# Optimization experiments

Hardware: AMD Instinct MI355X
Metric: run time of the kernel (lower is better)

## Reference

```python
import jax, jax.numpy as jnp
import numpy as np

IN_C = 256
QK_C = IN_C // 8  # 32
B, H, W = 8, 64, 64


def setup_inputs() -> dict:
    key = jax.random.key(0)
    ks = jax.random.split(key, 8)
    s_in = 1.0 / np.sqrt(IN_C)
    return {
        "x": jax.random.normal(ks[0], (B, IN_C, H, W), dtype=jnp.float32),
        "Wq": jax.random.normal(ks[1], (QK_C, IN_C), dtype=jnp.float32) * s_in,
        "bq": jax.random.normal(ks[2], (QK_C,), dtype=jnp.float32) * 0.01,
        "Wk": jax.random.normal(ks[3], (QK_C, IN_C), dtype=jnp.float32) * s_in,
        "bk": jax.random.normal(ks[4], (QK_C,), dtype=jnp.float32) * 0.01,
        "Wv": jax.random.normal(ks[5], (IN_C, IN_C), dtype=jnp.float32) * s_in,
        "bv": jax.random.normal(ks[6], (IN_C,), dtype=jnp.float32) * 0.01,
        # gamma is init to zero in the module, but use nonzero so output depends on attention
        "gamma": jnp.full((1,), 0.5, dtype=jnp.float32),
    }


def reference(x, Wq, bq, Wk, bk, Wv, bv, gamma):
    b, c, h, w = x.shape
    n = h * w
    xf = x.reshape(b, c, n)  # [B, C, N]
    # 1x1 convs == per-pixel linear projections over channels
    q = jnp.einsum('dc,bcn->bdn', Wq, xf) + bq[None, :, None]  # [B, C//8, N]
    k = jnp.einsum('dc,bcn->bdn', Wk, xf) + bk[None, :, None]  # [B, C//8, N]
    v = jnp.einsum('oc,bcn->bon', Wv, xf) + bv[None, :, None]  # [B, C, N]
    # attention_map[b, m, n'] = softmax_n'( q[b,:,m] . k[b,:,n'] )
    scores = jnp.einsum('bdm,bdn->bmn', q, k)  # [B, N, N]
    attn = jax.nn.softmax(scores, axis=-1)
    # out[b,c,m] = sum_n v[b,c,n] * attn[b,m,n]
    out = jnp.einsum('bcn,bmn->bcm', v, attn).reshape(b, c, h, w)
    return gamma * out + x
```

## Files before the change

### kernel.cpp

```cpp
#include <hip/hip_runtime.h>
#include <cstdint>

typedef __bf16 bf16x8 __attribute__((ext_vector_type(8)));
typedef float f32x16 __attribute__((ext_vector_type(16)));

#define LOG2E 1.44269504088896340736f

static __device__ __forceinline__ ushort f2bf(float f) {
  uint u = __builtin_bit_cast(uint, f);
  u = u + 0x7FFFu + ((u >> 16) & 1u);
  return (ushort)(u >> 16);
}

static __device__ __forceinline__ uint cvtpk_bf16(float lo, float hi) {
  uint r;
  asm("v_cvt_pk_bf16_f32 %0, %1, %2" : "=v"(r) : "v"(lo), "v"(hi));
  return r;
}

static __device__ __forceinline__ void plswap(uint& a, uint& b) {
  asm("v_permlane32_swap_b32 %0, %1" : "+v"(a), "+v"(b));
}

static __device__ __forceinline__ void gload16(const ushort* g, ushort* l) {
  __builtin_amdgcn_global_load_lds(
      (const __attribute__((address_space(1))) void*)g,
      (__attribute__((address_space(3))) void*)l, 16, 0, 0);
}

#if __has_builtin(__builtin_amdgcn_exp2f)
#define EXP2(x) __builtin_amdgcn_exp2f(x)
#else
#define EXP2(x) exp2f(x)
#endif


__global__ __launch_bounds__(256, 2) void proj_qkv(
    const float* __restrict__ x,
    const float* __restrict__ Wq, const float* __restrict__ bq,
    const float* __restrict__ Wk, const float* __restrict__ bk,
    const float* __restrict__ Wv, const float* __restrict__ bv,
    ushort* __restrict__ qo, ushort* __restrict__ ko, ushort* __restrict__ vo)
{
  __shared__ __align__(16) union SM {
    ushort xc[2][8192];
    ushort qT[256 * 40];
  } sm;

  const int tid = threadIdx.x;
  const int nt = blockIdx.x, b = blockIdx.y, dt = blockIdx.z;
  const int n0 = nt * 256;
  const int wv = tid >> 6, lane = tid & 63;
  const int l31 = lane & 31, hi = lane >> 5;
  const int dh = wv & 1, nh = wv >> 1;

  const float* wrow;
  float wsc = 1.0f;
  if (dt == 0) {
    if (dh == 0) { wrow = Wq + (size_t)l31 * 256; wsc = LOG2E; }
    else         { wrow = Wk + (size_t)l31 * 256; }
  } else {
    wrow = Wv + (size_t)((dt - 1) * 64 + dh * 32 + l31) * 256;
  }
  bf16x8 wf[16];
#pragma unroll
  for (int s = 0; s < 16; ++s) {
    float4 a = *(const float4*)(wrow + s * 16 + 8 * hi);
    float4 c = *(const float4*)(wrow + s * 16 + 8 * hi + 4);
    union { uint u[4]; bf16x8 v; } t;
    t.u[0] = cvtpk_bf16(a.x * wsc, a.y * wsc);
    t.u[1] = cvtpk_bf16(a.z * wsc, a.w * wsc);
    t.u[2] = cvtpk_bf16(c.x * wsc, c.y * wsc);
    t.u[3] = cvtpk_bf16(c.z * wsc, c.w * wsc);
    wf[s] = t.v;
  }

  f32x16 acc[4];
#pragma unroll
  for (int Tl = 0; Tl < 4; ++Tl)
#pragma unroll
    for (int r = 0; r < 16; ++r) acc[Tl][r] = 0.f;

  const float* xb = x + (size_t)b * 256 * 4096;

  const int o = wv, qd = lane;
  float4 xr[8];

  auto XLOAD = [&](int kc) {
    const float* src = xb + (size_t)(kc * 32 + 8 * o) * 4096 + n0 + 4 * qd;
#pragma unroll
    for (int j = 0; j < 8; ++j) xr[j] = *(const float4*)(src + (size_t)j * 4096);
  };
  auto XWRITE = [&](int buf) {
    const int base = (qd >> 3) * 1024 + (o >> 1) * 512 + (o & 1) * 256 + (qd & 7) * 32;
    const int xsw = (qd & 6) << 2;
#pragma unroll
    for (int e = 0; e < 4; ++e) {
      uint4 w;
      w.x = cvtpk_bf16(xr[0][e], xr[1][e]);
      w.y = cvtpk_bf16(xr[2][e], xr[3][e]);
      w.z = cvtpk_bf16(xr[4][e], xr[5][e]);
      w.w = cvtpk_bf16(xr[6][e], xr[7][e]);
      *(uint4*)&sm.xc[buf][(base + e * 8) ^ xsw] = w;
    }
  };

  const int rdoff = (lane * 8) ^ (((l31 >> 2) & 6) << 2);

  XLOAD(0);
  asm volatile("s_waitcnt vmcnt(0)" ::: "memory");
  XWRITE(0);
  __syncthreads();

  for (int kc = 0; kc < 8; ++kc) {
    if (kc < 7) XLOAD(kc + 1);
    const ushort* buf = sm.xc[kc & 1];
#pragma unroll
    for (int s2 = 0; s2 < 2; ++s2) {
#pragma unroll
      for (int Tl = 0; Tl < 4; ++Tl) {
        const int T = nh * 4 + Tl;
        bf16x8 a = *(const bf16x8*)&buf[T * 1024 + s2 * 512 + rdoff];
        if (s2 == 0)
          acc[Tl] = __builtin_amdgcn_mfma_f32_32x32x16_bf16(a, wf[kc * 2 + 0], acc[Tl], 0, 0, 0);
        else
          acc[Tl] = __builtin_amdgcn_mfma_f32_32x32x16_bf16(a, wf[kc * 2 + 1], acc[Tl], 0, 0, 0);
      }
    }
    if (kc < 7) {
      asm volatile("s_waitcnt vmcnt(0)" ::: "memory");
      XWRITE((kc + 1) & 1);
    }
    __syncthreads();
  }

  if (dt == 0) {
    if (dh == 0) {
      const float bq_ = bq[l31] * LOG2E;
#pragma unroll
      for (int Tl = 0; Tl < 4; ++Tl)
#pragma unroll
        for (int r = 0; r < 16; ++r) {
          int nl = (nh * 4 + Tl) * 32 + (r & 3) + 8 * (r >> 2) + 4 * hi;
          sm.qT[nl * 40 + l31] = f2bf(acc[Tl][r] + bq_);
        }
    } else {
      const float bk_ = bk[l31];
      const int kd = l31;
      const size_t kzb = (size_t)b * 131072;
      const size_t dbase = (size_t)(kd >> 4) * 512 + ((kd >> 3) & 1) * 256 + (kd & 7);
#pragma unroll
      for (int Tl = 0; Tl < 4; ++Tl) {
        const size_t Tg = (size_t)(nt * 8 + nh * 4 + Tl);
#pragma unroll
        for (int r = 0; r < 16; ++r) {
          int n31 = (r & 3) + 8 * (r >> 2) + 4 * hi;
          ko[kzb + Tg * 1024 + dbase + (size_t)n31 * 8] = f2bf(acc[Tl][r] + bk_);
        }
      }
    }
    __syncthreads();
    {
      ushort* dst = qo + (size_t)b * 131072 + (size_t)(n0 + tid) * 32;
#pragma unroll
      for (int i = 0; i < 4; ++i)
        *(uint4*)(dst + i * 8) = *(const uint4*)&sm.qT[tid * 40 + i * 8];
    }
  } else {
    const float bv_ = bv[(dt - 1) * 64 + dh * 32 + l31];
    const int cu = (dt - 1) * 2 + dh;
    const size_t vzb = (size_t)b * 1048576;
#pragma unroll
    for (int Tl = 0; Tl < 4; ++Tl) {
      const size_t Tg = (size_t)(nt * 8 + nh * 4 + Tl);
#pragma unroll
      for (int g = 0; g < 4; ++g) {
        ushort4 w;
        w.x = f2bf(acc[Tl][g * 4 + 0] + bv_);
        w.y = f2bf(acc[Tl][g * 4 + 1] + bv_);
        w.z = f2bf(acc[Tl][g * 4 + 2] + bv_);
        w.w = f2bf(acc[Tl][g * 4 + 3] + bv_);
        size_t addr = vzb + Tg * 8192 + (size_t)(cu * 2 + (g >> 1)) * 512
                      + (size_t)(g & 1) * 256 + (size_t)l31 * 8 + 4 * hi;
        *(ushort4*)(vo + addr) = w;
      }
    }
  }
}

static __device__ __forceinline__ float softmax_pack_only(
    f32x16& s, float& mrun, float& lsum, bf16x8& pb0o, bf16x8& pb1o)
{
  float pm = s[0];
#pragma unroll
  for (int r = 1; r < 16; ++r) pm = fmaxf(pm, s[r]);
  pm = fmaxf(pm, __shfl_xor(pm, 32));

  float aa = 1.0f;
  if (!__all(pm <= mrun + 8.0f)) {
    float mnew = fmaxf(mrun, pm);
    aa = EXP2(mrun - mnew);
    mrun = mnew;
    lsum *= aa;
  }

  float p[16];
  float ps = 0.f;
#pragma unroll
  for (int r = 0; r < 16; ++r) { p[r] = EXP2(s[r] - mrun); ps += p[r]; }
  ps += __shfl_xor(ps, 32);
  lsum += ps;

  uint pw[8];
#pragma unroll
  for (int j = 0; j < 8; ++j) pw[j] = cvtpk_bf16(p[2 * j], p[2 * j + 1]);
  plswap(pw[0], pw[2]); plswap(pw[1], pw[3]);
  plswap(pw[4], pw[6]); plswap(pw[5], pw[7]);
  union { uint u[4]; bf16x8 v; } pb0u, pb1u;
  pb0u.u[0] = pw[0]; pb0u.u[1] = pw[1]; pb0u.u[2] = pw[2]; pb0u.u[3] = pw[3];
  pb1u.u[0] = pw[4]; pb1u.u[1] = pw[5]; pb1u.u[2] = pw[6]; pb1u.u[3] = pw[7];
  pb0o = pb0u.v; pb1o = pb1u.v;
  return aa;
}

__global__ __launch_bounds__(512, 2) void attn_fused(
    const ushort* __restrict__ qs, const ushort* __restrict__ kz,
    const ushort* __restrict__ vz, const float* __restrict__ x,
    const float* __restrict__ gamma, float* __restrict__ out)
{
  __shared__ __align__(16) union SMem {
    ushort vbuf[8][2][2048];
    float  xch[4][2][2][16][64];
  } sm;
  __shared__ __align__(16) ushort kbuf[2][4][1024];
  __shared__ uint  pexch[2][2][4][64][8];
  __shared__ float afac[2][2][4][64];
  __shared__ float mlbuf[2][4][2][64];

  const int wg = blockIdx.x;
  const int swz = (wg & 7) * 32 + (wg >> 3);
  const int b = swz >> 5, mt = swz & 31;
  const int tid = threadIdx.x;
  const int wv = tid >> 6, lane = tid & 63;
  const int kh = wv >> 2, q = wv & 3;
  const int l31 = lane & 31, hi = lane >> 5;
  const int mbase = mt * 128;
  const int mSelf = mbase + q * 32 + l31;

  const ushort* qrow = qs + (size_t)b * 131072 + (size_t)mSelf * 32;
  bf16x8 qf0 = *(const bf16x8*)(qrow + 8 * hi);
  bf16x8 qf1 = *(const bf16x8*)(qrow + 16 + 8 * hi);

  const ushort* kb = kz + (size_t)b * 131072 + (size_t)kh * 64 * 1024;
  const ushort* vb = vz + (size_t)b * 1048576 + (size_t)kh * 64 * 8192;

  f32x16 acc[4][2];
#pragma unroll
  for (int mu = 0; mu < 4; ++mu)
#pragma unroll
    for (int cf = 0; cf < 2; ++cf)
#pragma unroll
      for (int r = 0; r < 16; ++r) acc[mu][cf][r] = 0.f;

  const f32x16 fzero = {};
  float mrun = -1e30f, lsum = 0.f;

  const int pswz = (lane * 8) ^ (lane & 4);

  auto ISSUE_V = [&](int t, int par) {
#pragma unroll
    for (int i = 0; i < 4; ++i)
      gload16(vb + (size_t)t * 8192 + (size_t)(q * 4 + i) * 512 + lane * 8,
              &sm.vbuf[wv][par][i * 512]);
  };
  auto ISSUE_K = [&](int t) {
    if (q < 2)
      gload16(kb + (size_t)t * 1024 + (size_t)q * 512 + lane * 8,
              &kbuf[kh][t & 3][q * 512]);
  };

  ISSUE_V(0, 0);
  ISSUE_K(0);
  ISSUE_K(1);
  ISSUE_V(1, 1);
  ISSUE_K(2);
  if (q < 2) { asm volatile("s_waitcnt vmcnt(5)" ::: "memory"); }
  else       { asm volatile("s_waitcnt vmcnt(4)" ::: "memory"); }
  __builtin_amdgcn_s_barrier();

#define BODY(T, W01, W23)                                                      \
  {                                                                            \
    const int t_ = (T);                                                        \
    const int vpar = t_ & 1, kslot = t_ & 3, xpar = t_ & 1;                    \
    if (q < 2) { asm volatile("s_waitcnt vmcnt(" #W01 ")" ::: "memory"); }     \
    else       { asm volatile("s_waitcnt vmcnt(" #W23 ")" ::: "memory"); }     \
                                                          \
    bf16x8 ka0 = *(const bf16x8*)&kbuf[kh][kslot][lane * 8];                   \
    bf16x8 ka1 = *(const bf16x8*)&kbuf[kh][kslot][512 + lane * 8];             \
    f32x16 s = __builtin_amdgcn_mfma_f32_32x32x16_bf16(ka0, qf0, fzero, 0, 0, 0); \
    s = __builtin_amdgcn_mfma_f32_32x32x16_bf16(ka1, qf1, s, 0, 0, 0);         \
    bf16x8 pbS0, pbS1;                                                         \
    float aa = softmax_pack_only(s, mrun, lsum, pbS0, pbS1);                   \
    { union { bf16x8 v; uint4 u; } c0, c1; c0.v = pbS0; c1.v = pbS1;           \
      uint* pp = &pexch[kh][xpar][q][0][0];                                    \
      *(uint4*)(pp + pswz) = c0.u;                                             \
      *(uint4*)(pp + (pswz ^ 4)) = c1.u; }                                     \
    afac[kh][xpar][q][lane] = aa;                                              \
    asm volatile("s_waitcnt lgkmcnt(0)" ::: "memory");                         \
    __builtin_amdgcn_s_barrier();                                              \
                                      \
    bf16x8 va0 = *(const bf16x8*)&sm.vbuf[wv][vpar][0 * 512 + lane * 8];       \
    bf16x8 va1 = *(const bf16x8*)&sm.vbuf[wv][vpar][1 * 512 + lane * 8];       \
    bf16x8 va2 = *(const bf16x8*)&sm.vbuf[wv][vpar][2 * 512 + lane * 8];       \
    bf16x8 va3 = *(const bf16x8*)&sm.vbuf[wv][vpar][3 * 512 + lane * 8];       \
    _Pragma("unroll")                                                          \
    for (int mu = 0; mu < 4; ++mu) {                                           \
      float aaU = afac[kh][xpar][mu][lane];                                    \
      uint* pr = &pexch[kh][xpar][mu][0][0];                                   \
      union { uint4 u; bf16x8 v; } r0, r1;                                     \
      r0.u = *(const uint4*)(pr + pswz);                                       \
      r1.u = *(const uint4*)(pr + (pswz ^ 4));                                 \
      if (!__all(aaU == 1.0f)) {                                               \
        _Pragma("unroll")                                                      \
        for (int cf = 0; cf < 2; ++cf)                                         \
          _Pragma("unroll")                                                    \
          for (int r = 0; r < 16; ++r) acc[mu][cf][r] *= aaU;                  \
      }                                                                        \
      __builtin_amdgcn_s_setprio(1);                                           \
      acc[mu][0] = __builtin_amdgcn_mfma_f32_32x32x16_bf16(va0, r0.v, acc[mu][0], 0, 0, 0); \
      acc[mu][0] = __builtin_amdgcn_mfma_f32_32x32x16_bf16(va1, r1.v, acc[mu][0], 0, 0, 0); \
      acc[mu][1] = __builtin_amdgcn_mfma_f32_32x32x16_bf16(va2, r0.v, acc[mu][1], 0, 0, 0); \
      acc[mu][1] = __builtin_amdgcn_mfma_f32_32x32x16_bf16(va3, r1.v, acc[mu][1], 0, 0, 0); \
      __builtin_amdgcn_s_setprio(0);                                           \
    }                                                                          \
    if (t_ < 62) ISSUE_V(t_ + 2, vpar);                                        \
    if (t_ < 61) ISSUE_K(t_ + 3);                                              \
  }

  for (int t = 0; t < 62; ++t) BODY(t, 5, 4);
  BODY(62, 4, 4);
  BODY(63, 0, 0);
#undef BODY

  mlbuf[kh][q][0][lane] = mrun;
  mlbuf[kh][q][1][lane] = lsum;
  asm volatile("s_waitcnt lgkmcnt(0)" ::: "memory");
  __builtin_amdgcn_s_barrier();

  const float g = gamma[0];
  const float* xc = x + (size_t)b * 256 * 4096;
  float* oc = out + (size_t)b * 256 * 4096;

  if (kh == 1) {
#pragma unroll
    for (int mu = 0; mu < 2; ++mu)
#pragma unroll
      for (int cf = 0; cf < 2; ++cf)
#pragma unroll
        for (int r = 0; r < 16; ++r)
          sm.xch[q][mu][cf][r][lane] = acc[mu][cf][r];
  }
  asm volatile("s_waitcnt lgkmcnt(0)" ::: "memory");
  __builtin_amdgcn_s_barrier();
  if (kh == 0) {
#pragma unroll
    for (int mu = 0; mu < 2; ++mu) {
      float m0 = mlbuf[0][mu][0][lane], l0 = mlbuf[0][mu][1][lane];
      float m1 = mlbuf[1][mu][0][lane], l1 = mlbuf[1][mu][1][lane];
      float ms = fmaxf(m0, m1);
      float w0 = EXP2(m0 - ms), w1 = EXP2(m1 - ms);
      float inv = 1.0f / (l0 * w0 + l1 * w1);
      int m = mbase + mu * 32 + l31;
#pragma unroll
      for (int cf = 0; cf < 2; ++cf)
#pragma unroll
        for (int r = 0; r < 16; ++r) {
          float val = acc[mu][cf][r] * w0 + sm.xch[q][mu][cf][r][lane] * w1;
          int c = q * 64 + cf * 32 + (r & 3) + 8 * (r >> 2) + 4 * hi;
          oc[(size_t)c * 4096 + m] = g * (val * inv) + xc[(size_t)c * 4096 + m];
        }
    }
  }
  __builtin_amdgcn_s_barrier();
  if (kh == 1) {
#pragma unroll
    for (int mu = 0; mu < 2; ++mu)
#pragma unroll
      for (int cf = 0; cf < 2; ++cf)
#pragma unroll
        for (int r = 0; r < 16; ++r)
          sm.xch[q][mu][cf][r][lane] = acc[2 + mu][cf][r];
  }
  asm volatile("s_waitcnt lgkmcnt(0)" ::: "memory");
  __builtin_amdgcn_s_barrier();
  if (kh == 0) {
#pragma unroll
    for (int mu = 0; mu < 2; ++mu) {
      float m0 = mlbuf[0][2 + mu][0][lane], l0 = mlbuf[0][2 + mu][1][lane];
      float m1 = mlbuf[1][2 + mu][0][lane], l1 = mlbuf[1][2 + mu][1][lane];
      float ms = fmaxf(m0, m1);
      float w0 = EXP2(m0 - ms), w1 = EXP2(m1 - ms);
      float inv = 1.0f / (l0 * w0 + l1 * w1);
      int m = mbase + (2 + mu) * 32 + l31;
#pragma unroll
      for (int cf = 0; cf < 2; ++cf)
#pragma unroll
        for (int r = 0; r < 16; ++r) {
          float val = acc[2 + mu][cf][r] * w0 + sm.xch[q][mu][cf][r][lane] * w1;
          int c = q * 64 + cf * 32 + (r & 3) + 8 * (r >> 2) + 4 * hi;
          oc[(size_t)c * 4096 + m] = g * (val * inv) + xc[(size_t)c * 4096 + m];
        }
    }
  }
}

extern "C" void kernel_launch(void* const* d_in, const int* in_sizes, int n_in,
                              void* d_out, int out_size, void* d_ws, size_t ws_size,
                              hipStream_t stream) {
  const float* x  = (const float*)d_in[0];
  const float* Wq = (const float*)d_in[1];
  const float* bq = (const float*)d_in[2];
  const float* Wk = (const float*)d_in[3];
  const float* bk = (const float*)d_in[4];
  const float* Wv = (const float*)d_in[5];
  const float* bv = (const float*)d_in[6];
  const float* gm = (const float*)d_in[7];
  float* out = (float*)d_out;

  ushort* qs = (ushort*)d_ws;
  ushort* kzp = qs + (size_t)8 * 131072;
  ushort* vzp = kzp + (size_t)8 * 131072;

  proj_qkv<<<dim3(16, 8, 5), 256, 0, stream>>>(x, Wq, bq, Wk, bk, Wv, bv, qs, kzp, vzp);
  attn_fused<<<dim3(256), 512, 0, stream>>>(qs, kzp, vzp, x, gm, out);
}
```

Baseline: 138.7 us.

## Software-pipeline PV of previous tile with QK softmax of current tile

Restructures the attention loop so each iteration computes the QK scores for tile t and then runs the PV matmul for tile t-1, before the softmax of tile t. This overlaps the softmax's exp/ALU work and barrier latency with MFMA work from the previous tile, collapsing to one barrier per iteration. The V prefetch distance shrinks from two tiles ahead to one, the vmcnt waits are retuned, and sched_barriers are added to pin the instruction order. The risk is that the shorter V prefetch exposes load latency, and the fixed scheduling may block useful compiler reordering.

```diff
diff --git a/kernel.cpp b/kernel.cpp
--- a/kernel.cpp
+++ b/kernel.cpp
@@ -279,44 +279,24 @@
               &kbuf[kh][t & 3][q * 512]);
   };
 
-  ISSUE_V(0, 0);
   ISSUE_K(0);
   ISSUE_K(1);
-  ISSUE_V(1, 1);
+  ISSUE_V(0, 0);
   ISSUE_K(2);
-  if (q < 2) { asm volatile("s_waitcnt vmcnt(5)" ::: "memory"); }
-  else       { asm volatile("s_waitcnt vmcnt(4)" ::: "memory"); }
+  if (q < 2) { asm volatile("s_waitcnt vmcnt(1)" ::: "memory"); }
   __builtin_amdgcn_s_barrier();
-
-#define BODY(T, W01, W23)                                                      \
+  __builtin_amdgcn_sched_barrier(0);
+
+#define PV_PREV(SLOT)                                                          \
   {                                                                            \
-    const int t_ = (T);                                                        \
-    const int vpar = t_ & 1, kslot = t_ & 3, xpar = t_ & 1;                    \
-    if (q < 2) { asm volatile("s_waitcnt vmcnt(" #W01 ")" ::: "memory"); }     \
-    else       { asm volatile("s_waitcnt vmcnt(" #W23 ")" ::: "memory"); }     \
-                                                          \
-    bf16x8 ka0 = *(const bf16x8*)&kbuf[kh][kslot][lane * 8];                   \
-    bf16x8 ka1 = *(const bf16x8*)&kbuf[kh][kslot][512 + lane * 8];             \
-    f32x16 s = __builtin_amdgcn_mfma_f32_32x32x16_bf16(ka0, qf0, fzero, 0, 0, 0); \
-    s = __builtin_amdgcn_mfma_f32_32x32x16_bf16(ka1, qf1, s, 0, 0, 0);         \
-    bf16x8 pbS0, pbS1;                                                         \
-    float aa = softmax_pack_only(s, mrun, lsum, pbS0, pbS1);                   \
-    { union { bf16x8 v; uint4 u; } c0, c1; c0.v = pbS0; c1.v = pbS1;           \
-      uint* pp = &pexch[kh][xpar][q][0][0];                                    \
-      *(uint4*)(pp + pswz) = c0.u;                                             \
-      *(uint4*)(pp + (pswz ^ 4)) = c1.u; }                                     \
-    afac[kh][xpar][q][lane] = aa;                                              \
-    asm volatile("s_waitcnt lgkmcnt(0)" ::: "memory");                         \
-    __builtin_amdgcn_s_barrier();                                              \
-                                      \
-    bf16x8 va0 = *(const bf16x8*)&sm.vbuf[wv][vpar][0 * 512 + lane * 8];       \
-    bf16x8 va1 = *(const bf16x8*)&sm.vbuf[wv][vpar][1 * 512 + lane * 8];       \
-    bf16x8 va2 = *(const bf16x8*)&sm.vbuf[wv][vpar][2 * 512 + lane * 8];       \
-    bf16x8 va3 = *(const bf16x8*)&sm.vbuf[wv][vpar][3 * 512 + lane * 8];       \
+    bf16x8 va0 = *(const bf16x8*)&sm.vbuf[wv][SLOT][0 * 512 + lane * 8];       \
+    bf16x8 va1 = *(const bf16x8*)&sm.vbuf[wv][SLOT][1 * 512 + lane * 8];       \
+    bf16x8 va2 = *(const bf16x8*)&sm.vbuf[wv][SLOT][2 * 512 + lane * 8];       \
+    bf16x8 va3 = *(const bf16x8*)&sm.vbuf[wv][SLOT][3 * 512 + lane * 8];       \
     _Pragma("unroll")                                                          \
     for (int mu = 0; mu < 4; ++mu) {                                           \
-      float aaU = afac[kh][xpar][mu][lane];                                    \
-      uint* pr = &pexch[kh][xpar][mu][0][0];                                   \
+      float aaU = afac[kh][SLOT][mu][lane];                                    \
+      uint* pr = &pexch[kh][SLOT][mu][0][0];                                   \
       union { uint4 u; bf16x8 v; } r0, r1;                                     \
       r0.u = *(const uint4*)(pr + pswz);                                       \
       r1.u = *(const uint4*)(pr + (pswz ^ 4));                                 \
@@ -333,19 +313,50 @@
       acc[mu][1] = __builtin_amdgcn_mfma_f32_32x32x16_bf16(va3, r1.v, acc[mu][1], 0, 0, 0); \
       __builtin_amdgcn_s_setprio(0);                                           \
     }                                                                          \
-    if (t_ < 62) ISSUE_V(t_ + 2, vpar);                                        \
-    if (t_ < 61) ISSUE_K(t_ + 3);                                              \
-  }
-
-  for (int t = 0; t < 62; ++t) BODY(t, 5, 4);
-  BODY(62, 4, 4);
-  BODY(63, 0, 0);
+  }
+
+#define BODY(T, W01, W23, DO_PV)                                               \
+  {                                                                            \
+    const int t_ = (T);                                                        \
+    const int kslot = t_ & 3, xpar = t_ & 1, slotP = (t_ ^ 1) & 1;             \
+    if (q < 2) { asm volatile("s_waitcnt vmcnt(" #W01 ")" ::: "memory"); }     \
+    else       { asm volatile("s_waitcnt vmcnt(" #W23 ")" ::: "memory"); }     \
+                               \
+    bf16x8 ka0 = *(const bf16x8*)&kbuf[kh][kslot][lane * 8];                   \
+    bf16x8 ka1 = *(const bf16x8*)&kbuf[kh][kslot][512 + lane * 8];             \
+    f32x16 s = __builtin_amdgcn_mfma_f32_32x32x16_bf16(ka0, qf0, fzero, 0, 0, 0); \
+    s = __builtin_amdgcn_mfma_f32_32x32x16_bf16(ka1, qf1, s, 0, 0, 0);         \
+        \
+    if (DO_PV) PV_PREV(slotP);                                                 \
+    bf16x8 pbS0, pbS1;                                                         \
+    float aa = softmax_pack_only(s, mrun, lsum, pbS0, pbS1);                   \
+    { union { bf16x8 v; uint4 u; } c0, c1; c0.v = pbS0; c1.v = pbS1;           \
+      uint* pp = &pexch[kh][xpar][q][0][0];                                    \
+      *(uint4*)(pp + pswz) = c0.u;                                             \
+      *(uint4*)(pp + (pswz ^ 4)) = c1.u; }                                     \
+    afac[kh][xpar][q][lane] = aa;                                              \
+    asm volatile("s_waitcnt lgkmcnt(0)" ::: "memory");                         \
+    __builtin_amdgcn_s_barrier();                                              \
+    __builtin_amdgcn_sched_barrier(0);                                         \
+          \
+    if (t_ <= 62) ISSUE_V(t_ + 1, slotP);                                      \
+    if (t_ <= 60) ISSUE_K(t_ + 3);                                             \
+  }
+
+  BODY(0, 20, 20, false);
+  for (int t = 1; t < 62; ++t) BODY(t, 5, 4, true);
+  BODY(62, 4, 4, true);
+  BODY(63, 4, 4, true);
 #undef BODY
+  asm volatile("s_waitcnt vmcnt(0)" ::: "memory");
+  PV_PREV(1);
+#undef PV_PREV
 
   mlbuf[kh][q][0][lane] = mrun;
   mlbuf[kh][q][1][lane] = lsum;
   asm volatile("s_waitcnt lgkmcnt(0)" ::: "memory");
   __builtin_amdgcn_s_barrier();
+  __builtin_amdgcn_sched_barrier(0);
 
   const float g = gamma[0];
   const float* xc = x + (size_t)b * 256 * 4096;
@@ -362,6 +373,7 @@
   }
   asm volatile("s_waitcnt lgkmcnt(0)" ::: "memory");
   __builtin_amdgcn_s_barrier();
+  __builtin_amdgcn_sched_barrier(0);
   if (kh == 0) {
 #pragma unroll
     for (int mu = 0; mu < 2; ++mu) {
@@ -382,6 +394,7 @@
     }
   }
   __builtin_amdgcn_s_barrier();
+  __builtin_amdgcn_sched_barrier(0);
   if (kh == 1) {
 #pragma unroll
     for (int mu = 0; mu < 2; ++mu)
@@ -393,6 +406,7 @@
   }
   asm volatile("s_waitcnt lgkmcnt(0)" ::: "memory");
   __builtin_amdgcn_s_barrier();
+  __builtin_amdgcn_sched_barrier(0);
   if (kh == 0) {
 #pragma unroll
     for (int mu = 0; mu < 2; ++mu) {
```

Measured after the change: 150.8 us. 1.09x slower.

## Split attention across key halves into separate blocks with global merge kernel

Applied to the files above, without the earlier changes.

Instead of one 512-thread block covering both key halves and merging through shared memory, the attention is split into 512 blocks of 256 threads, each handling one key half for 128 queries. Partial outputs are written to global memory (fp32 for half 0 into the output buffer, bf16 for half 1 into workspace) along with running max and sum, and a separate merge kernel combines them with the residual. This aims at better occupancy and scheduling flexibility. In exchange it adds an extra launch and a large global round-trip of partial results, and rounds one partial to bf16. The old fused path is kept as a fallback when the workspace is too small.

```diff
diff --git a/kernel.cpp b/kernel.cpp
--- a/kernel.cpp
+++ b/kernel.cpp
@@ -10,6 +10,11 @@
   uint u = __builtin_bit_cast(uint, f);
   u = u + 0x7FFFu + ((u >> 16) & 1u);
   return (ushort)(u >> 16);
+}
+
+static __device__ __forceinline__ float bf2f(ushort s) {
+  uint u = ((uint)s) << 16;
+  return __builtin_bit_cast(float, u);
 }
 
 static __device__ __forceinline__ uint cvtpk_bf16(float lo, float hi) {
@@ -221,6 +226,186 @@
   pb1u.u[0] = pw[4]; pb1u.u[1] = pw[5]; pb1u.u[2] = pw[6]; pb1u.u[3] = pw[7];
   pb0o = pb0u.v; pb1o = pb1u.v;
   return aa;
+}
+
+__global__ __launch_bounds__(256, 2) void attn_split(
+    const ushort* __restrict__ qs, const ushort* __restrict__ kz,
+    const ushort* __restrict__ vz, float* __restrict__ outp,
+    ushort* __restrict__ pws, float* __restrict__ mw, float* __restrict__ lw)
+{
+  __shared__ __align__(16) ushort vbuf[4][2][2048];
+  __shared__ __align__(16) ushort kbuf[4][1024];
+  __shared__ uint  pexch[2][4][64][8];
+  __shared__ float afac[2][4][64];
+
+  const int wg = blockIdx.x;
+  const int swz = (wg & 7) * 64 + (wg >> 3);
+  const int b = swz >> 6;
+  const int r6 = swz & 63;
+  const int kh = r6 >> 5, mt = r6 & 31;
+  const int tid = threadIdx.x;
+  const int q = tid >> 6, lane = tid & 63;
+  const int l31 = lane & 31, hi = lane >> 5;
+  const int mbase = mt * 128;
+  const int mSelf = mbase + q * 32 + l31;
+
+  const ushort* qrow = qs + (size_t)b * 131072 + (size_t)mSelf * 32;
+  bf16x8 qf0 = *(const bf16x8*)(qrow + 8 * hi);
+  bf16x8 qf1 = *(const bf16x8*)(qrow + 16 + 8 * hi);
+
+  const ushort* kb = kz + (size_t)b * 131072 + (size_t)kh * 64 * 1024;
+  const ushort* vb = vz + (size_t)b * 1048576 + (size_t)kh * 64 * 8192;
+
+  f32x16 acc[4][2];
+#pragma unroll
+  for (int mu = 0; mu < 4; ++mu)
+#pragma unroll
+    for (int cf = 0; cf < 2; ++cf)
+#pragma unroll
+      for (int r = 0; r < 16; ++r) acc[mu][cf][r] = 0.f;
+
+  const f32x16 fzero = {};
+  float mrun = -1e30f, lsum = 0.f;
+
+  const int pswz = (lane * 8) ^ (lane & 4);
+
+  auto ISSUE_V = [&](int t, int par) {
+#pragma unroll
+    for (int i = 0; i < 4; ++i)
+      gload16(vb + (size_t)t * 8192 + (size_t)(q * 4 + i) * 512 + lane * 8,
+              &vbuf[q][par][i * 512]);
+  };
+  auto ISSUE_K = [&](int t) {
+    if (q < 2)
+      gload16(kb + (size_t)t * 1024 + (size_t)q * 512 + lane * 8,
+              &kbuf[t & 3][q * 512]);
+  };
+
+  ISSUE_V(0, 0);
+  ISSUE_K(0);
+  ISSUE_K(1);
+  ISSUE_V(1, 1);
+  ISSUE_K(2);
+  if (q < 2) { asm volatile("s_waitcnt vmcnt(5)" ::: "memory"); }
+  else       { asm volatile("s_waitcnt vmcnt(4)" ::: "memory"); }
+  __builtin_amdgcn_s_barrier();
+
+#define BODY(T, W01, W23)                                                      \
+  {                                                                            \
+    const int t_ = (T);                                                        \
+    const int vpar = t_ & 1, kslot = t_ & 3, xpar = t_ & 1;                    \
+    if (q < 2) { asm volatile("s_waitcnt vmcnt(" #W01 ")" ::: "memory"); }     \
+    else       { asm volatile("s_waitcnt vmcnt(" #W23 ")" ::: "memory"); }     \
+    bf16x8 ka0 = *(const bf16x8*)&kbuf[kslot][lane * 8];                       \
+    bf16x8 ka1 = *(const bf16x8*)&kbuf[kslot][512 + lane * 8];                 \
+    f32x16 s = __builtin_amdgcn_mfma_f32_32x32x16_bf16(ka0, qf0, fzero, 0, 0, 0); \
+    s = __builtin_amdgcn_mfma_f32_32x32x16_bf16(ka1, qf1, s, 0, 0, 0);         \
+    bf16x8 pbS0, pbS1;                                                         \
+    float aa = softmax_pack_only(s, mrun, lsum, pbS0, pbS1);                   \
+    { union { bf16x8 v; uint4 u; } c0, c1; c0.v = pbS0; c1.v = pbS1;           \
+      uint* pp = &pexch[xpar][q][0][0];                                        \
+      *(uint4*)(pp + pswz) = c0.u;                                             \
+      *(uint4*)(pp + (pswz ^ 4)) = c1.u; }                                     \
+    afac[xpar][q][lane] = aa;                                                  \
+    asm volatile("s_waitcnt lgkmcnt(0)" ::: "memory");                         \
+    __builtin_amdgcn_s_barrier();                                              \
+    bf16x8 va0 = *(const bf16x8*)&vbuf[q][vpar][0 * 512 + lane * 8];           \
+    bf16x8 va1 = *(const bf16x8*)&vbuf[q][vpar][1 * 512 + lane * 8];           \
+    bf16x8 va2 = *(const bf16x8*)&vbuf[q][vpar][2 * 512 + lane * 8];           \
+    bf16x8 va3 = *(const bf16x8*)&vbuf[q][vpar][3 * 512 + lane * 8];           \
+    _Pragma("unroll")                                                          \
+    for (int mu = 0; mu < 4; ++mu) {                                           \
+      float aaU = afac[xpar][mu][lane];                                        \
+      uint* pr = &pexch[xpar][mu][0][0];                                       \
+      union { uint4 u; bf16x8 v; } r0, r1;                                     \
+      r0.u = *(const uint4*)(pr + pswz);                                       \
+      r1.u = *(const uint4*)(pr + (pswz ^ 4));                                 \
+      if (!__all(aaU == 1.0f)) {                                               \
+        _Pragma("unroll")                                                      \
+        for (int cf = 0; cf < 2; ++cf)                                         \
+          _Pragma("unroll")                                                    \
+          for (int r = 0; r < 16; ++r) acc[mu][cf][r] *= aaU;                  \
+      }                                                                        \
+      __builtin_amdgcn_s_setprio(1);                                           \
+      acc[mu][0] = __builtin_amdgcn_mfma_f32_32x32x16_bf16(va0, r0.v, acc[mu][0], 0, 0, 0); \
+      acc[mu][0] = __builtin_amdgcn_mfma_f32_32x32x16_bf16(va1, r1.v, acc[mu][0], 0, 0, 0); \
+      acc[mu][1] = __builtin_amdgcn_mfma_f32_32x32x16_bf16(va2, r0.v, acc[mu][1], 0, 0, 0); \
+      acc[mu][1] = __builtin_amdgcn_mfma_f32_32x32x16_bf16(va3, r1.v, acc[mu][1], 0, 0, 0); \
+      __builtin_amdgcn_s_setprio(0);                                           \
+    }                                                                          \
+    if (t_ < 62) ISSUE_V(t_ + 2, vpar);                                        \
+    if (t_ < 61) ISSUE_K(t_ + 3);                                              \
+  }
+
+  for (int t = 0; t < 62; ++t) BODY(t, 5, 4);
+  BODY(62, 4, 4);
+  BODY(63, 0, 0);
+#undef BODY
+
+  if (lane < 32) {
+    const size_t mli = ((size_t)kh * 8 + b) * 4096 + mbase + q * 32 + l31;
+    mw[mli] = mrun;
+    lw[mli] = lsum;
+  }
+  if (kh == 0) {
+    float* op = outp + (size_t)b * 1048576;
+#pragma unroll
+    for (int mu = 0; mu < 4; ++mu)
+#pragma unroll
+      for (int cf = 0; cf < 2; ++cf)
+#pragma unroll
+        for (int r = 0; r < 16; ++r) {
+          int c = q * 64 + cf * 32 + (r & 3) + 8 * (r >> 2) + 4 * hi;
+          int m = mbase + mu * 32 + l31;
+          op[(size_t)c * 4096 + m] = acc[mu][cf][r];
+        }
+  } else {
+    ushort* pp = pws + (size_t)b * 1048576;
+#pragma unroll
+    for (int mu = 0; mu < 4; ++mu)
+#pragma unroll
+      for (int cf = 0; cf < 2; ++cf)
+#pragma unroll
+        for (int r = 0; r < 16; ++r) {
+          int c = q * 64 + cf * 32 + (r & 3) + 8 * (r >> 2) + 4 * hi;
+          int m = mbase + mu * 32 + l31;
+          pp[(size_t)c * 4096 + m] = f2bf(acc[mu][cf][r]);
+        }
+  }
+}
+
+__global__ __launch_bounds__(256, 4) void merge_split(
+    const ushort* __restrict__ pws, const float* __restrict__ mw,
+    const float* __restrict__ lw, const float* __restrict__ x,
+    const float* __restrict__ gamma, float* __restrict__ out)
+{
+  const float g = gamma[0];
+  const int nf4 = 8 * 256 * 1024;
+  for (int i4 = blockIdx.x * 256 + threadIdx.x; i4 < nf4; i4 += gridDim.x * 256) {
+    const int m4 = i4 & 1023;
+    const int bc = i4 >> 10;
+    const int b = bc >> 8;
+    const size_t base = (size_t)bc * 4096 + (size_t)m4 * 4;
+    float4 a0 = *(const float4*)(out + base);
+    ushort4 a1 = *(const ushort4*)(pws + base);
+    float4 xv = *(const float4*)(x + base);
+    const size_t mb = (size_t)b * 4096 + (size_t)m4 * 4;
+    float a0f[4] = {a0.x, a0.y, a0.z, a0.w};
+    float a1f[4] = {bf2f(a1.x), bf2f(a1.y), bf2f(a1.z), bf2f(a1.w)};
+    float xf[4] = {xv.x, xv.y, xv.z, xv.w};
+    float res[4];
+#pragma unroll
+    for (int j = 0; j < 4; ++j) {
+      float m0 = mw[mb + j], m1 = mw[mb + j + 32768];
+      float l0 = lw[mb + j], l1 = lw[mb + j + 32768];
+      float ms = fmaxf(m0, m1);
+      float w0 = EXP2(m0 - ms), w1 = EXP2(m1 - ms);
+      float inv = 1.0f / (l0 * w0 + l1 * w1);
+      res[j] = g * ((a0f[j] * w0 + a1f[j] * w1) * inv) + xf[j];
+    }
+    float4 o; o.x = res[0]; o.y = res[1]; o.z = res[2]; o.w = res[3];
+    *(float4*)(out + base) = o;
+  }
 }
 
 __global__ __launch_bounds__(512, 2) void attn_fused(
@@ -294,7 +479,6 @@
     const int vpar = t_ & 1, kslot = t_ & 3, xpar = t_ & 1;                    \
     if (q < 2) { asm volatile("s_waitcnt vmcnt(" #W01 ")" ::: "memory"); }     \
     else       { asm volatile("s_waitcnt vmcnt(" #W23 ")" ::: "memory"); }     \
-                                                          \
     bf16x8 ka0 = *(const bf16x8*)&kbuf[kh][kslot][lane * 8];                   \
     bf16x8 ka1 = *(const bf16x8*)&kbuf[kh][kslot][512 + lane * 8];             \
     f32x16 s = __builtin_amdgcn_mfma_f32_32x32x16_bf16(ka0, qf0, fzero, 0, 0, 0); \
@@ -308,7 +492,6 @@
     afac[kh][xpar][q][lane] = aa;                                              \
     asm volatile("s_waitcnt lgkmcnt(0)" ::: "memory");                         \
     __builtin_amdgcn_s_barrier();                                              \
-                                      \
     bf16x8 va0 = *(const bf16x8*)&sm.vbuf[wv][vpar][0 * 512 + lane * 8];       \
     bf16x8 va1 = *(const bf16x8*)&sm.vbuf[wv][vpar][1 * 512 + lane * 8];       \
     bf16x8 va2 = *(const bf16x8*)&sm.vbuf[wv][vpar][2 * 512 + lane * 8];       \
@@ -382,7 +565,15 @@
     }
   }
   __builtin_amdgcn_s_barrier();
-  if (kh == 1) {
+  if (kh == 0) {
+#pragma unroll
+    for (int mu = 0; mu < 2; ++mu)
+#pragma unroll
+      for (int cf = 0; cf < 2; ++cf)
+#pragma unroll
+        for (int r = 0; r < 16; ++r)
+          ;
+  } else {
 #pragma unroll
     for (int mu = 0; mu < 2; ++mu)
 #pragma unroll
@@ -432,5 +623,18 @@
   ushort* vzp = kzp + (size_t)8 * 131072;
 
   proj_qkv<<<dim3(16, 8, 5), 256, 0, stream>>>(x, Wq, bq, Wk, bk, Wv, bv, qs, kzp, vzp);
-  attn_fused<<<dim3(256), 512, 0, stream>>>(qs, kzp, vzp, x, gm, out);
-}
+
+  const size_t NEED = 20971520ull
+                    + 16777216ull
+                    + 262144ull
+                    + 262144ull;
+  if (ws_size >= NEED) {
+    ushort* pws = vzp + (size_t)8 * 1048576;
+    float* mw = (float*)(pws + (size_t)8 * 1048576);
+    float* lw = mw + (size_t)2 * 8 * 4096;
+    attn_split<<<dim3(512), 256, 0, stream>>>(qs, kzp, vzp, out, pws, mw, lw);
+    merge_split<<<dim3(2048), 256, 0, stream>>>(pws, mw, lw, x, gm, out);
+  } else {
+    attn_fused<<<dim3(256), 512, 0, stream>>>(qs, kzp, vzp, x, gm, out);
+  }
+}
```

New measurement: 151.7 us. 9.3% more time.
